# Kernel optimization log

Hardware: AMD Instinct MI355X
Metric: run time of the kernel (lower is better)

Reference implementation:

```python
import jax, jax.numpy as jnp
import numpy as np

HID = 512      # LSTM hidden per direction (1024 // 2)
EMB = 768      # BERT hidden size
NUM_TAG = 9
B, S = 64, 512


def setup_inputs() -> dict:
    key = jax.random.key(0)
    ks = jax.random.split(key, 12)
    g = lambda k, sh, sc: (jax.random.normal(k, sh, jnp.float32) * sc)
    return {
        "x": jax.random.normal(ks[0], (B, S, EMB), jnp.float32),
        "mask": jnp.ones((B, S), jnp.int32),
        "target_tag": jax.random.randint(ks[1], (B, S), 0, NUM_TAG, jnp.int32),
        "w_ih_f": g(ks[2], (4 * HID, EMB), 0.02),
        "w_hh_f": g(ks[3], (4 * HID, HID), 0.02),
        "b_f": jnp.zeros((4 * HID,), jnp.float32),
        "w_ih_b": g(ks[4], (4 * HID, EMB), 0.02),
        "w_hh_b": g(ks[5], (4 * HID, HID), 0.02),
        "b_b": jnp.zeros((4 * HID,), jnp.float32),
        "w_out": g(ks[6], (NUM_TAG, 2 * HID), 0.02),
        "b_out": jnp.zeros((NUM_TAG,), jnp.float32),
        "start_trans": g(ks[7], (NUM_TAG,), 0.1),
        "end_trans": g(ks[8], (NUM_TAG,), 0.1),
        "trans": g(ks[9], (NUM_TAG, NUM_TAG), 0.1),
    }


def _lstm_dir(x, w_ih, w_hh, b, reverse):
    # x: [B,S,E] -> outputs [S,B,H]; PyTorch gate order i,f,g,o
    xp = jnp.einsum('bse,ge->sbg', x, w_ih) + b  # precompute input proj [S,B,4H]
    if reverse:
        xp = xp[::-1]
    Bq = x.shape[0]
    def step(carry, xt):
        h, c = carry
        pre = xt + h @ w_hh.T
        i, f, g_, o = jnp.split(pre, 4, axis=-1)
        c = jax.nn.sigmoid(f) * c + jax.nn.sigmoid(i) * jnp.tanh(g_)
        h = jax.nn.sigmoid(o) * jnp.tanh(c)
        return (h, c), h
    init = (jnp.zeros((Bq, HID), x.dtype), jnp.zeros((Bq, HID), x.dtype))
    _, hs = jax.lax.scan(step, init, xp)
    if reverse:
        hs = hs[::-1]
    return hs


def _crf_nll_token_mean(emis, tags, m, start_trans, end_trans, trans):
    # emis: [S,B,T] time-major; tags: [S,B] int; m: [S,B] float (mask)
    Sq, Bq, T = emis.shape
    bidx = jnp.arange(Bq)
    # ---- numerator: score of the gold path ----
    num = start_trans[tags[0]] + emis[0, bidx, tags[0]]
    trans_steps = trans[tags[:-1], tags[1:]]                                   # [S-1,B]
    emit_steps = jnp.take_along_axis(emis[1:], tags[1:, :, None], axis=2)[..., 0]
    num = num + ((trans_steps + emit_steps) * m[1:]).sum(0)
    last_idx = m.sum(0).astype(jnp.int32) - 1                                   # [B]
    num = num + end_trans[tags[last_idx, bidx]]
    # ---- denominator: forward algorithm (log-sum-exp recursion) ----
    alpha0 = start_trans + emis[0]                                              # [B,T]
    def step(alpha, em):
        emis_t, m_t = em
        nxt = jax.nn.logsumexp(alpha[:, :, None] + trans[None] + emis_t[:, None, :], axis=1)
        return jnp.where(m_t[:, None] > 0, nxt, alpha), None
    alpha, _ = jax.lax.scan(step, alpha0, (emis[1:], m[1:]))
    den = jax.nn.logsumexp(alpha + end_trans, axis=1)
    llh = num - den
    return -(llh.sum() / m.sum())  # reduction='token_mean', negated (model loss)


def reference(x, mask, target_tag, w_ih_f, w_hh_f, b_f, w_ih_b, w_hh_b, b_b,
              w_out, b_out, start_trans, end_trans, trans):
    hf = _lstm_dir(x, w_ih_f, w_hh_f, b_f, reverse=False)   # [S,B,H]
    hb = _lstm_dir(x, w_ih_b, w_hh_b, b_b, reverse=True)    # [S,B,H]
    h = jnp.concatenate([hf, hb], axis=-1)                  # [S,B,2H]
    emis = jnp.einsum('sbh,th->sbt', h, w_out) + b_out      # [S,B,T] (dropout=identity in eval)
    tags = target_tag.T                                     # [S,B]
    m = mask.T.astype(emis.dtype)                           # [S,B]
    return _crf_nll_token_mean(emis, tags, m, start_trans, end_trans, trans)
```

## Files before the change

kernel.cpp:

```cpp
#include <hip/hip_runtime.h>
#include <cstdint>
#include <cstddef>

#define SS   512
#define BB   64
#define EMBD 768
#define HIDN 512
#define G4   2048
#define NTAG 9

typedef __attribute__((ext_vector_type(8))) __bf16 bf16x8;
typedef __attribute__((ext_vector_type(4))) float  f32x4;
typedef unsigned long long u64;

union HCast { f32x4 f; bf16x8 h; };
union UCast { f32x4 f; unsigned u[4]; };

__device__ inline void load_h16_bypass(const void* base, f32x4* f) {
  asm volatile(
    "global_load_dwordx4 %0, %16, off sc0 sc1\n\t"
    "global_load_dwordx4 %1, %16, off offset:64 sc0 sc1\n\t"
    "global_load_dwordx4 %2, %16, off offset:128 sc0 sc1\n\t"
    "global_load_dwordx4 %3, %16, off offset:192 sc0 sc1\n\t"
    "global_load_dwordx4 %4, %16, off offset:256 sc0 sc1\n\t"
    "global_load_dwordx4 %5, %16, off offset:320 sc0 sc1\n\t"
    "global_load_dwordx4 %6, %16, off offset:384 sc0 sc1\n\t"
    "global_load_dwordx4 %7, %16, off offset:448 sc0 sc1\n\t"
    "global_load_dwordx4 %8, %16, off offset:512 sc0 sc1\n\t"
    "global_load_dwordx4 %9, %16, off offset:576 sc0 sc1\n\t"
    "global_load_dwordx4 %10, %16, off offset:640 sc0 sc1\n\t"
    "global_load_dwordx4 %11, %16, off offset:704 sc0 sc1\n\t"
    "global_load_dwordx4 %12, %16, off offset:768 sc0 sc1\n\t"
    "global_load_dwordx4 %13, %16, off offset:832 sc0 sc1\n\t"
    "global_load_dwordx4 %14, %16, off offset:896 sc0 sc1\n\t"
    "global_load_dwordx4 %15, %16, off offset:960 sc0 sc1\n\t"
    "s_waitcnt vmcnt(0)"
    : "=&v"(f[0]), "=&v"(f[1]), "=&v"(f[2]), "=&v"(f[3]),
      "=&v"(f[4]), "=&v"(f[5]), "=&v"(f[6]), "=&v"(f[7]),
      "=&v"(f[8]), "=&v"(f[9]), "=&v"(f[10]), "=&v"(f[11]),
      "=&v"(f[12]), "=&v"(f[13]), "=&v"(f[14]), "=&v"(f[15])
    : "v"(base)
    : "memory");
}
__device__ inline void store_h8_bypass(void* p, u64 v) {
  asm volatile("global_store_dwordx2 %0, %1, off sc0 sc1" :: "v"(p), "v"(v) : "memory");
}
__device__ inline void store_i32_bypass(int* p, int v) {
  asm volatile("global_store_dword %0, %1, off sc0 sc1" :: "v"(p), "v"(v) : "memory");
}
__device__ inline int load_i32_bypass(const int* p) {
  int v;
  asm volatile("global_load_dword %0, %1, off sc0 sc1\n\ts_waitcnt vmcnt(0)"
               : "=v"(v) : "v"(p) : "memory");
  return v;
}

__global__ __launch_bounds__(256) void cvt_kernel(
    const float* __restrict__ src, __bf16* __restrict__ dst, int n8)
{
  int i = blockIdx.x * 256 + threadIdx.x;
  if (i >= n8) return;
  f32x4 a = *reinterpret_cast<const f32x4*>(src + 8 * (size_t)i);
  f32x4 b = *reinterpret_cast<const f32x4*>(src + 8 * (size_t)i + 4);
  bf16x8 o;
  o[0]=(__bf16)a[0]; o[1]=(__bf16)a[1]; o[2]=(__bf16)a[2]; o[3]=(__bf16)a[3];
  o[4]=(__bf16)b[0]; o[5]=(__bf16)b[1]; o[6]=(__bf16)b[2]; o[7]=(__bf16)b[3];
  *reinterpret_cast<bf16x8*>(dst + 8 * (size_t)i) = o;
}

__global__ __launch_bounds__(256, 2) void proj_kernel(
    const __bf16* __restrict__ xb, const __bf16* __restrict__ wfb,
    const __bf16* __restrict__ wbb, const float* __restrict__ bias_f,
    const float* __restrict__ bias_b, float* __restrict__ xp,
    int t0, int chunk)
{
  const int nb = blockIdx.x;
  const int tt = blockIdx.y;
  const int d  = blockIdx.z;
  const int s  = d ? (SS - 1 - (t0 + tt)) : (t0 + tt);
  const __bf16* __restrict__ wih = d ? wbb : wfb;
  const float*  __restrict__ bias = d ? bias_b : bias_f;

  const int t = threadIdx.x, wv = t >> 6, l = t & 63;
  const int quad = l >> 4, col = l & 15;

  const __bf16* brow[8];
  float bj[8];
  const int pbase = 128 * nb;
#pragma unroll
  for (int j = 0; j < 8; j++) {
    int p    = pbase + 16 * j + col;
    int gate = p & 3;
    int hc   = 16 * (p >> 6) + 4 * ((p >> 2) & 3) + ((p >> 4) & 3);
    int g    = gate * HIDN + hc;
    brow[j]  = wih + (size_t)g * EMBD + 8 * quad;
    bj[j]    = bias[g];
  }
  const __bf16* arow = xb + ((size_t)(16 * wv + col) * SS + s) * EMBD + 8 * quad;

  f32x4 acc[8];
#pragma unroll
  for (int j = 0; j < 8; j++) acc[j] = f32x4{0.f, 0.f, 0.f, 0.f};

  for (int kk = 0; kk < 24; kk++) {
    bf16x8 a = *reinterpret_cast<const bf16x8*>(arow + 32 * kk);
#pragma unroll
    for (int j = 0; j < 8; j++) {
      bf16x8 b = *reinterpret_cast<const bf16x8*>(brow[j] + 32 * kk);
      acc[j] = __builtin_amdgcn_mfma_f32_16x16x32_bf16(a, b, acc[j], 0, 0, 0);
    }
  }
  float* xpd = xp + (size_t)(d * chunk + tt) * (size_t)G4 * BB + 16 * wv + 4 * quad;
#pragma unroll
  for (int j = 0; j < 8; j++) {
    int p = pbase + 16 * j + col;
    f32x4 v = acc[j];
    v[0] += bj[j]; v[1] += bj[j]; v[2] += bj[j]; v[3] += bj[j];
    *reinterpret_cast<f32x4*>(xpd + (size_t)p * BB) = v;
  }
}

struct RecCtl {
  int prog[2][64];
  int pad[128];
};

struct RecParams {
  const float* xp;
  const float* whh_f;
  const float* whh_b;
  __bf16* hh;
  float*  cT;
  RecCtl* ctl;
  int     chunk;
};

__global__ __launch_bounds__(256, 1) void rec_kernel(RecParams p)
{
  const int wg   = blockIdx.x;
  const int d    = wg >> 5;
  const int sl   = wg & 31;
  const int t    = threadIdx.x;
  const int wv   = t >> 6;
  const int l    = t & 63;
  const int quad = l >> 4;
  const int col  = l & 15;
  const int hcl  = col >> 2;
  const int gate = col & 3;
  const int j4   = col & 3;

  const size_t slotsz = (size_t)BB * HIDN;

  {
    const size_t qper = (size_t)p.chunk * slotsz / 4;
    const size_t totq = 2 * qper;
    const size_t gtid = (size_t)wg * 256 + t;
    for (size_t q = gtid; q < totq; q += (size_t)64 * 256) {
      const size_t dd  = q / qper;
      const size_t off = q - dd * qper;
      char* dst = (char*)p.hh + (dd * (p.chunk + 1) + 1) * slotsz * 2 + off * 8;
      store_h8_bypass(dst, 0xFFFFFFFFFFFFFFFFull);
    }
    __builtin_amdgcn_s_waitcnt(0);
    __syncthreads();
    if (t == 0) store_i32_bypass(&p.ctl->prog[0][wg], 1);
    if (wv == 0) {
      const int* slot = &p.ctl->prog[0][l];
      while (true) {
        int v = load_i32_bypass(slot);
        if (__ballot(v != 0) == ~0ull) break;
        __builtin_amdgcn_s_sleep(1);
      }
    }
    __syncthreads();
  }

  const float* __restrict__ whh = d ? p.whh_b : p.whh_f;

  bf16x8 bfrag[4][16];
#pragma unroll
  for (int j = 0; j < 4; j++) {
    const int hcb = 16 * sl + 4 * hcl + j;
    const float* wr = whh + (size_t)(gate * HIDN + hcb) * HIDN + 8 * quad;
#pragma unroll
    for (int kk = 0; kk < 16; kk++) {
      f32x4 w0 = *reinterpret_cast<const f32x4*>(wr + 32 * kk);
      f32x4 w1 = *reinterpret_cast<const f32x4*>(wr + 32 * kk + 4);
      bf16x8 v;
      v[0] = (__bf16)w0[0]; v[1] = (__bf16)w0[1]; v[2] = (__bf16)w0[2]; v[3] = (__bf16)w0[3];
      v[4] = (__bf16)w1[0]; v[5] = (__bf16)w1[1]; v[6] = (__bf16)w1[2]; v[7] = (__bf16)w1[3];
      bfrag[j][kk] = v;
    }
  }

  const int bA = 16 * wv + col;
  const int bC = 16 * wv + 4 * quad + gate;
  const int hcs = 16 * sl + 4 * hcl;
  __bf16* hhd = p.hh + (size_t)d * (p.chunk + 1) * slotsz;
  const float* xpd = p.xp + (size_t)d * p.chunk * ((size_t)G4 * BB);

  float c[4];
#pragma unroll
  for (int j = 0; j < 4; j++)
    c[j] = p.cT[((size_t)d * HIDN + hcs + j) * BB + bC];

  f32x4 xpn[4];
#pragma unroll
  for (int j = 0; j < 4; j++)
    xpn[j] = *reinterpret_cast<const f32x4*>(
        xpd + (size_t)(64 * sl + 16 * j + col) * BB + 16 * wv + 4 * quad);

  u64 hword = 0;
  for (int tt = 0; tt < p.chunk; tt++) {
    const char* hbase = (const char*)hhd + (size_t)tt * slotsz * 2
                      + (size_t)bA * (HIDN * 2) + quad * 16;
    f32x4 araw[16];
    for (;;) {
      load_h16_bypass(hbase, araw);
      unsigned mx = 0u;
#pragma unroll
      for (int kk = 0; kk < 16; kk++) {
        UCast q; q.f = araw[kk];
        unsigned a01 = q.u[0] > q.u[1] ? q.u[0] : q.u[1];
        unsigned a23 = q.u[2] > q.u[3] ? q.u[2] : q.u[3];
        unsigned am  = a01 > a23 ? a01 : a23;
        mx = mx > am ? mx : am;
      }
      if (__all(mx != 0xFFFFFFFFu)) break;
      __builtin_amdgcn_s_sleep(1);
    }
    bf16x8 afrag[16];
#pragma unroll
    for (int kk = 0; kk < 16; kk++) { HCast hc_; hc_.f = araw[kk]; afrag[kk] = hc_.h; }

    f32x4 acc[4][2];
#pragma unroll
    for (int j = 0; j < 4; j++) {
      acc[j][0] = xpn[j];
      acc[j][1] = f32x4{0.f, 0.f, 0.f, 0.f};
    }
#pragma unroll
    for (int kk = 0; kk < 16; kk += 2) {
#pragma unroll
      for (int j = 0; j < 4; j++) {
        acc[j][0] = __builtin_amdgcn_mfma_f32_16x16x32_bf16(afrag[kk],     bfrag[j][kk],     acc[j][0], 0, 0, 0);
        acc[j][1] = __builtin_amdgcn_mfma_f32_16x16x32_bf16(afrag[kk + 1], bfrag[j][kk + 1], acc[j][1], 0, 0, 0);
      }
    }

    hword = 0;
#pragma unroll
    for (int j = 0; j < 4; j++) {
      float v0 = acc[j][0][0] + acc[j][1][0];
      float v1 = acc[j][0][1] + acc[j][1][1];
      float v2 = acc[j][0][2] + acc[j][1][2];
      float v3 = acc[j][0][3] + acc[j][1][3];
      {
        float t0 = __shfl_xor(v1, 1); float t1 = __shfl_xor(v0, 1);
        float t2 = __shfl_xor(v3, 1); float t3 = __shfl_xor(v2, 1);
        if (j4 & 1) { v0 = t0; v2 = t2; } else { v1 = t1; v3 = t3; }
        float u0 = __shfl_xor(v2, 2); float u1 = __shfl_xor(v3, 2);
        float u2 = __shfl_xor(v0, 2); float u3 = __shfl_xor(v1, 2);
        if (j4 & 2) { v0 = u0; v1 = u1; } else { v2 = u2; v3 = u3; }
      }
      float ig = 1.f / (1.f + __expf(-v0));
      float fg = 1.f / (1.f + __expf(-v1));
      float gg = 1.f - 2.f / (__expf(2.f * v2) + 1.f);
      float og = 1.f / (1.f + __expf(-v3));
      c[j] = fg * c[j] + ig * gg;
      float hn = og * (1.f - 2.f / (__expf(2.f * c[j]) + 1.f));
      union { __bf16 b; unsigned short u; } cv; cv.b = (__bf16)hn;
      hword |= (u64)cv.u << (16 * j);
    }
    store_h8_bypass((char*)hhd + (size_t)(tt + 1) * slotsz * 2
                    + (size_t)bC * (HIDN * 2) + (size_t)hcs * 2, hword);

    if (tt + 1 < p.chunk) {
#pragma unroll
      for (int j = 0; j < 4; j++)
        xpn[j] = *reinterpret_cast<const f32x4*>(
            xpd + (size_t)(tt + 1) * ((size_t)G4 * BB)
            + (size_t)(64 * sl + 16 * j + col) * BB + 16 * wv + 4 * quad);
    }
  }

  if (p.chunk == 1) {
    __builtin_amdgcn_s_waitcnt(0);
    __syncthreads();
    if (t == 0) store_i32_bypass(&p.ctl->prog[1][wg], 1);
    if (wv == 0) {
      const int* slot = &p.ctl->prog[1][l];
      while (true) {
        int v = load_i32_bypass(slot);
        if (__ballot(v != 0) == ~0ull) break;
        __builtin_amdgcn_s_sleep(1);
      }
    }
    __syncthreads();
  }

  store_h8_bypass((char*)hhd + (size_t)bC * (HIDN * 2) + (size_t)hcs * 2, hword);
#pragma unroll
  for (int j = 0; j < 4; j++)
    p.cT[((size_t)d * HIDN + hcs + j) * BB + bC] = c[j];
  __builtin_amdgcn_s_waitcnt(0);
}

__global__ __launch_bounds__(256) void emis_kernel(
    const __bf16* __restrict__ hh, const float* __restrict__ w_out,
    float* __restrict__ emis_f, float* __restrict__ emis_b,
    int t0, int chunk)
{
  const int tt = blockIdx.x;
  const int d  = blockIdx.y;
  const int t  = threadIdx.x;
  const int b  = t & 63;
  const int grp = t >> 6;

  const __bf16* hp = hh + ((size_t)d * (chunk + 1) + tt + 1) * ((size_t)BB * HIDN)
                   + (size_t)b * HIDN;
  const float* w0 = w_out + (size_t)grp * (2 * HIDN) + d * HIDN;
  const float* w1 = w_out + (size_t)(grp + 4) * (2 * HIDN) + d * HIDN;
  const float* w2 = w_out + (size_t)8 * (2 * HIDN) + d * HIDN;

  float a0 = 0.f, a1 = 0.f, a2 = 0.f;
  for (int k = 0; k < HIDN; k += 8) {
    bf16x8 hv8 = *reinterpret_cast<const bf16x8*>(hp + k);
#pragma unroll
    for (int j = 0; j < 8; j++) {
      float hv = (float)hv8[j];
      a0 += hv * w0[k + j];
      a1 += hv * w1[k + j];
      a2 += hv * w2[k + j];
    }
  }
  const int sidx = (d == 0) ? (t0 + tt) : (SS - 1 - (t0 + tt));
  float* dst = d ? emis_b : emis_f;
  dst[((size_t)sidx * BB + b) * NTAG + grp]     = a0;
  dst[((size_t)sidx * BB + b) * NTAG + grp + 4] = a1;
  if (grp == 0) dst[((size_t)sidx * BB + b) * NTAG + 8] = a2;
}

__global__ __launch_bounds__(64) void crf_kernel(
    const float* __restrict__ emis_f, const float* __restrict__ emis_b,
    const float* __restrict__ b_out, const float* __restrict__ start_tr,
    const float* __restrict__ end_tr, const float* __restrict__ trans,
    const int* __restrict__ mask, const int* __restrict__ target,
    float* __restrict__ llh)
{
  const int b    = blockIdx.x;
  const int lane = threadIdx.x;

  auto E = [&](int s, int tg) -> float {
    size_t o = ((size_t)s * BB + b) * NTAG + tg;
    return emis_f[o] + emis_b[o] + b_out[tg];
  };

  float numpart = 0.f;
  int msum = 0;
  for (int s = lane; s < SS; s += 64) {
    int m = mask[b * SS + s];
    msum += m;
    if (s >= 1 && m > 0) {
      int tp = target[b * SS + s - 1];
      int tc = target[b * SS + s];
      numpart += trans[tp * NTAG + tc] + E(s, tc);
    }
  }
#pragma unroll
  for (int off = 32; off > 0; off >>= 1) {
    numpart += __shfl_down(numpart, off, 64);
    msum    += __shfl_down(msum, off, 64);
  }

  const int tc = lane;
  const bool act = (tc < NTAG);
  float trc[NTAG] = {0.f};
  float alpha = 0.f;
  if (act) {
#pragma unroll
    for (int i = 0; i < NTAG; i++) trc[i] = trans[i * NTAG + tc];
    alpha = start_tr[tc] + E(0, tc);
  }
  for (int s = 1; s < SS; s++) {
    float e = act ? E(s, tc) : 0.f;
    float av[NTAG];
    float mx = -3.0e30f;
#pragma unroll
    for (int i = 0; i < NTAG; i++) {
      av[i] = __shfl(alpha, i, 64) + trc[i];
      mx = fmaxf(mx, av[i]);
    }
    float sum = 0.f;
#pragma unroll
    for (int i = 0; i < NTAG; i++) sum += __expf(av[i] - mx);
    float nxt = mx + __logf(sum) + e;
    if (act && mask[b * SS + s] > 0) alpha = nxt;
  }
  float fv = act ? (alpha + end_tr[tc]) : -3.0e30f;
  float q[NTAG];
  float mx2 = -3.0e30f;
#pragma unroll
  for (int i = 0; i < NTAG; i++) {
    q[i] = __shfl(fv, i, 64);
    mx2 = fmaxf(mx2, q[i]);
  }
  float s2 = 0.f;
#pragma unroll
  for (int i = 0; i < NTAG; i++) s2 += __expf(q[i] - mx2);
  float den = mx2 + __logf(s2);

  if (lane == 0) {
    int last = msum - 1;
    int tg0 = target[b * SS + 0];
    int tgl = target[b * SS + last];
    float num = start_tr[tg0] + E(0, tg0) + numpart + end_tr[tgl];
    llh[b] = num - den;
  }
}

__global__ __launch_bounds__(256) void fin_kernel(
    const float* __restrict__ llh, const int* __restrict__ mask,
    float* __restrict__ out)
{
  __shared__ float sf[256];
  __shared__ int   si[256];
  const int t = threadIdx.x;
  float a = (t < BB) ? llh[t] : 0.f;
  int m = 0;
  for (int i = t; i < BB * SS; i += 256) m += mask[i];
  sf[t] = a; si[t] = m;
  __syncthreads();
  for (int o = 128; o > 0; o >>= 1) {
    if (t < o) { sf[t] += sf[t + o]; si[t] += si[t + o]; }
    __syncthreads();
  }
  if (t == 0) out[0] = -(sf[0] / (float)si[0]);
}

extern "C" void kernel_launch(void* const* d_in, const int* in_sizes, int n_in,
                              void* d_out, int out_size, void* d_ws, size_t ws_size,
                              hipStream_t stream)
{
  const float* x     = (const float*)d_in[0];
  const int*   mask  = (const int*)d_in[1];
  const int*   targ  = (const int*)d_in[2];
  const float* wih_f = (const float*)d_in[3];
  const float* whh_f = (const float*)d_in[4];
  const float* b_f   = (const float*)d_in[5];
  const float* wih_b = (const float*)d_in[6];
  const float* whh_b = (const float*)d_in[7];
  const float* b_b   = (const float*)d_in[8];
  const float* w_out = (const float*)d_in[9];
  const float* b_out = (const float*)d_in[10];
  const float* st    = (const float*)d_in[11];
  const float* et    = (const float*)d_in[12];
  const float* tr    = (const float*)d_in[13];
  float* out = (float*)d_out;

  const size_t nxb   = (size_t)BB * SS * EMBD;
  const size_t nwb   = (size_t)G4 * EMBD;
  const size_t ctl_i = sizeof(RecCtl) / 4;
  const size_t fixed_f = (size_t)2 * SS * BB * NTAG + 64 + (size_t)2 * HIDN * BB
                       + ctl_i + nxb / 2 + nwb;
  int chunk = 1;
  for (int c = SS; c >= 1; c >>= 1) {
    size_t need = fixed_f * 4 + (size_t)c * 2 * G4 * BB * 4
                + (size_t)2 * (c + 1) * BB * HIDN * 2;
    if (need <= ws_size) { chunk = c; break; }
  }

  float* fp = (float*)d_ws;
  float* emis_f = fp; fp += (size_t)SS * BB * NTAG;
  float* emis_b = fp; fp += (size_t)SS * BB * NTAG;
  float* llh    = fp; fp += 64;
  float* cT     = fp; fp += (size_t)2 * HIDN * BB;
  RecCtl* ctl   = (RecCtl*)fp; fp += ctl_i;
  __bf16* xb16  = (__bf16*)fp; fp += nxb / 2;
  __bf16* wfb16 = (__bf16*)fp; fp += nwb / 2;
  __bf16* wbb16 = (__bf16*)fp; fp += nwb / 2;
  float* xp     = fp; fp += (size_t)chunk * 2 * G4 * BB;
  __bf16* hh    = (__bf16*)fp;

  {
    int n8 = (int)(nxb / 8);
    cvt_kernel<<<dim3((n8 + 255) / 256), 256, 0, stream>>>(x, xb16, n8);
    int w8 = (int)(nwb / 8);
    cvt_kernel<<<dim3((w8 + 255) / 256), 256, 0, stream>>>(wih_f, wfb16, w8);
    cvt_kernel<<<dim3((w8 + 255) / 256), 256, 0, stream>>>(wih_b, wbb16, w8);
  }

  const size_t slotsz = (size_t)BB * HIDN;
  hipMemsetAsync(cT, 0, (size_t)2 * HIDN * BB * sizeof(float), stream);
  hipMemsetAsync(hh, 0, slotsz * sizeof(__bf16), stream);
  hipMemsetAsync(hh + (size_t)(chunk + 1) * slotsz, 0, slotsz * sizeof(__bf16), stream);

  const int nch = SS / chunk;
  for (int c = 0; c < nch; c++) {
    const int t0 = c * chunk;
    hipMemsetAsync(ctl, 0, sizeof(RecCtl), stream);
    proj_kernel<<<dim3(16, chunk, 2), 256, 0, stream>>>(
        xb16, wfb16, wbb16, b_f, b_b, xp, t0, chunk);
    RecParams rp{xp, whh_f, whh_b, hh, cT, ctl, chunk};
    void* ka[] = {&rp};
    hipLaunchCooperativeKernel(rec_kernel, dim3(64), dim3(256), ka, 0, stream);
    emis_kernel<<<dim3(chunk, 2), 256, 0, stream>>>(
        hh, w_out, emis_f, emis_b, t0, chunk);
  }
  crf_kernel<<<dim3(64), 64, 0, stream>>>(emis_f, emis_b, b_out, st, et, tr, mask, targ, llh);
  fin_kernel<<<dim3(1), 256, 0, stream>>>(llh, mask, out);
}
```

Before: 5.216 ms.

## Merge recurrent slices into 512-thread blocks sharing polled h via LDS

The recurrent kernel now runs 32 workgroups of 512 threads instead of 64 of 256, so each workgroup handles two hidden-column slices. Only the first four waves poll global memory for the previous hidden state. They then pass it to the other four waves through a swizzled LDS buffer, and the grid barrier is cut to 32 flags. The aim is to halve the global polling and load traffic per step. In exchange, every timestep gains two block-wide barriers and an LDS round trip on the serial critical path.

```diff
diff --git a/kernel.cpp b/kernel.cpp
--- a/kernel.cpp
+++ b/kernel.cpp
@@ -16,7 +16,7 @@
 union HCast { f32x4 f; bf16x8 h; };
 union UCast { f32x4 f; unsigned u[4]; };
 
-__device__ inline void load_h16_bypass(const void* base, f32x4* f) {
+__device__ inline void load_h16_mall(const void* base, f32x4* f) {
   asm volatile(
     "global_load_dwordx4 %0, %16, off sc0 sc1\n\t"
     "global_load_dwordx4 %1, %16, off offset:64 sc0 sc1\n\t"
@@ -42,7 +42,7 @@
     : "v"(base)
     : "memory");
 }
-__device__ inline void store_h8_bypass(void* p, u64 v) {
+__device__ inline void store_h8_mall(void* p, u64 v) {
   asm volatile("global_store_dwordx2 %0, %1, off sc0 sc1" :: "v"(p), "v"(v) : "memory");
 }
 __device__ inline void store_i32_bypass(int* p, int v) {
@@ -135,39 +135,44 @@
   int     chunk;
 };
 
-__global__ __launch_bounds__(256, 1) void rec_kernel(RecParams p)
+__global__ __launch_bounds__(512, 2) void rec_kernel(RecParams p)
 {
   const int wg   = blockIdx.x;
-  const int d    = wg >> 5;
-  const int sl   = wg & 31;
+  const int d    = wg >> 4;
+  const int slw  = wg & 15;
   const int t    = threadIdx.x;
-  const int wv   = t >> 6;
+  const int w    = t >> 6;
+  const int ws2  = w >> 2;
+  const int wv   = w & 3;
   const int l    = t & 63;
   const int quad = l >> 4;
   const int col  = l & 15;
   const int hcl  = col >> 2;
   const int gate = col & 3;
   const int j4   = col & 3;
+  const int g    = 2 * slw + ws2;
 
   const size_t slotsz = (size_t)BB * HIDN;
+
+  __shared__ f32x4 hlds[256 * 16];
 
   {
     const size_t qper = (size_t)p.chunk * slotsz / 4;
     const size_t totq = 2 * qper;
-    const size_t gtid = (size_t)wg * 256 + t;
-    for (size_t q = gtid; q < totq; q += (size_t)64 * 256) {
+    const size_t gtid = (size_t)wg * 512 + t;
+    for (size_t q = gtid; q < totq; q += (size_t)32 * 512) {
       const size_t dd  = q / qper;
       const size_t off = q - dd * qper;
       char* dst = (char*)p.hh + (dd * (p.chunk + 1) + 1) * slotsz * 2 + off * 8;
-      store_h8_bypass(dst, 0xFFFFFFFFFFFFFFFFull);
+      store_h8_mall(dst, 0xFFFFFFFFFFFFFFFFull);
     }
     __builtin_amdgcn_s_waitcnt(0);
     __syncthreads();
     if (t == 0) store_i32_bypass(&p.ctl->prog[0][wg], 1);
-    if (wv == 0) {
+    if (w == 0) {
       const int* slot = &p.ctl->prog[0][l];
       while (true) {
-        int v = load_i32_bypass(slot);
+        int v = (l < 32) ? load_i32_bypass(slot) : 1;
         if (__ballot(v != 0) == ~0ull) break;
         __builtin_amdgcn_s_sleep(1);
       }
@@ -180,7 +185,7 @@
   bf16x8 bfrag[4][16];
 #pragma unroll
   for (int j = 0; j < 4; j++) {
-    const int hcb = 16 * sl + 4 * hcl + j;
+    const int hcb = 16 * g + 4 * hcl + j;
     const float* wr = whh + (size_t)(gate * HIDN + hcb) * HIDN + 8 * quad;
 #pragma unroll
     for (int kk = 0; kk < 16; kk++) {
@@ -195,7 +200,8 @@
 
   const int bA = 16 * wv + col;
   const int bC = 16 * wv + 4 * quad + gate;
-  const int hcs = 16 * sl + 4 * hcl;
+  const int hcs = 16 * g + 4 * hcl;
+  const int rowp = bA * 4 + quad;
   __bf16* hhd = p.hh + (size_t)d * (p.chunk + 1) * slotsz;
   const float* xpd = p.xp + (size_t)d * p.chunk * ((size_t)G4 * BB);
 
@@ -208,27 +214,40 @@
 #pragma unroll
   for (int j = 0; j < 4; j++)
     xpn[j] = *reinterpret_cast<const f32x4*>(
-        xpd + (size_t)(64 * sl + 16 * j + col) * BB + 16 * wv + 4 * quad);
+        xpd + (size_t)(64 * g + 16 * j + col) * BB + 16 * wv + 4 * quad);
 
   u64 hword = 0;
   for (int tt = 0; tt < p.chunk; tt++) {
-    const char* hbase = (const char*)hhd + (size_t)tt * slotsz * 2
-                      + (size_t)bA * (HIDN * 2) + quad * 16;
     f32x4 araw[16];
-    for (;;) {
-      load_h16_bypass(hbase, araw);
-      unsigned mx = 0u;
-#pragma unroll
-      for (int kk = 0; kk < 16; kk++) {
-        UCast q; q.f = araw[kk];
-        unsigned a01 = q.u[0] > q.u[1] ? q.u[0] : q.u[1];
-        unsigned a23 = q.u[2] > q.u[3] ? q.u[2] : q.u[3];
-        unsigned am  = a01 > a23 ? a01 : a23;
-        mx = mx > am ? mx : am;
+    if (ws2 == 0) {
+      const char* hbase = (const char*)hhd + (size_t)tt * slotsz * 2
+                        + (size_t)bA * (HIDN * 2) + quad * 16;
+      for (;;) {
+        load_h16_mall(hbase, araw);
+        unsigned mx = 0u;
+#pragma unroll
+        for (int kk = 0; kk < 16; kk++) {
+          UCast q; q.f = araw[kk];
+          unsigned a01 = q.u[0] > q.u[1] ? q.u[0] : q.u[1];
+          unsigned a23 = q.u[2] > q.u[3] ? q.u[2] : q.u[3];
+          unsigned am  = a01 > a23 ? a01 : a23;
+          mx = mx > am ? mx : am;
+        }
+        if (__all(mx != 0xFFFFFFFFu)) break;
+        __builtin_amdgcn_s_sleep(1);
       }
-      if (__all(mx != 0xFFFFFFFFu)) break;
-      __builtin_amdgcn_s_sleep(1);
-    }
+#pragma unroll
+      for (int kk = 0; kk < 16; kk++)
+        hlds[rowp * 16 + (kk ^ (rowp & 15))] = araw[kk];
+    }
+    __syncthreads();
+    if (ws2 == 1) {
+#pragma unroll
+      for (int kk = 0; kk < 16; kk++)
+        araw[kk] = hlds[rowp * 16 + (kk ^ (rowp & 15))];
+    }
+    __syncthreads();
+
     bf16x8 afrag[16];
 #pragma unroll
     for (int kk = 0; kk < 16; kk++) { HCast hc_; hc_.f = araw[kk]; afrag[kk] = hc_.h; }
@@ -272,15 +291,15 @@
       union { __bf16 b; unsigned short u; } cv; cv.b = (__bf16)hn;
       hword |= (u64)cv.u << (16 * j);
     }
-    store_h8_bypass((char*)hhd + (size_t)(tt + 1) * slotsz * 2
-                    + (size_t)bC * (HIDN * 2) + (size_t)hcs * 2, hword);
+    store_h8_mall((char*)hhd + (size_t)(tt + 1) * slotsz * 2
+                  + (size_t)bC * (HIDN * 2) + (size_t)hcs * 2, hword);
 
     if (tt + 1 < p.chunk) {
 #pragma unroll
       for (int j = 0; j < 4; j++)
         xpn[j] = *reinterpret_cast<const f32x4*>(
             xpd + (size_t)(tt + 1) * ((size_t)G4 * BB)
-            + (size_t)(64 * sl + 16 * j + col) * BB + 16 * wv + 4 * quad);
+            + (size_t)(64 * g + 16 * j + col) * BB + 16 * wv + 4 * quad);
     }
   }
 
@@ -288,10 +307,10 @@
     __builtin_amdgcn_s_waitcnt(0);
     __syncthreads();
     if (t == 0) store_i32_bypass(&p.ctl->prog[1][wg], 1);
-    if (wv == 0) {
+    if (w == 0) {
       const int* slot = &p.ctl->prog[1][l];
       while (true) {
-        int v = load_i32_bypass(slot);
+        int v = (l < 32) ? load_i32_bypass(slot) : 1;
         if (__ballot(v != 0) == ~0ull) break;
         __builtin_amdgcn_s_sleep(1);
       }
@@ -299,7 +318,7 @@
     __syncthreads();
   }
 
-  store_h8_bypass((char*)hhd + (size_t)bC * (HIDN * 2) + (size_t)hcs * 2, hword);
+  store_h8_mall((char*)hhd + (size_t)bC * (HIDN * 2) + (size_t)hcs * 2, hword);
 #pragma unroll
   for (int j = 0; j < 4; j++)
     p.cT[((size_t)d * HIDN + hcs + j) * BB + bC] = c[j];
@@ -503,7 +522,7 @@
         xb16, wfb16, wbb16, b_f, b_b, xp, t0, chunk);
     RecParams rp{xp, whh_f, whh_b, hh, cT, ctl, chunk};
     void* ka[] = {&rp};
-    hipLaunchCooperativeKernel(rec_kernel, dim3(64), dim3(256), ka, 0, stream);
+    hipLaunchCooperativeKernel(rec_kernel, dim3(32), dim3(512), ka, 0, stream);
     emis_kernel<<<dim3(chunk, 2), 256, 0, stream>>>(
         hh, w_out, emis_f, emis_b, t0, chunk);
   }
```

After: 9.401 ms. 1.8x slower.
